# Kernel optimization log

Measured on AMD Instinct MI355X. Metric: run time of the kernel, lower is better.

Reference implementation:

```python
import jax, jax.numpy as jnp
import numpy as np

N, D, E, C = 8192, 64, 524288, 2


def setup_inputs() -> dict:
    key = jax.random.key(0)
    ks = jax.random.split(key, 14)
    src = jax.random.randint(ks[0], (E,), 0, N, dtype=jnp.int32)
    dst = jax.random.randint(ks[1], (E,), 0, N, dtype=jnp.int32)
    h = jax.random.normal(ks[2], (N, D), jnp.float32)
    # dense adjacency consistent with the edge list (A[u,v]=1 for edge u->v)
    one = jnp.ones((E,), jnp.float32)
    A = jnp.zeros((N, N), jnp.float32).at[src, dst].max(one)
    # motif adjacencies: random subsets of the base edges
    keep1 = jax.random.bernoulli(ks[3], 0.5, (E,)).astype(jnp.float32)
    keep2 = jax.random.bernoulli(ks[4], 0.3, (E,)).astype(jnp.float32)
    A1 = jnp.zeros((N, N), jnp.float32).at[src, dst].max(keep1)
    A2 = jnp.zeros((N, N), jnp.float32).at[src, dst].max(keep2)
    s = 0.05
    Ww = jax.random.normal(ks[5], (D, D), jnp.float32) * s
    Wb = jax.random.normal(ks[6], (D,), jnp.float32) * s
    fc0 = jax.random.normal(ks[7], (D, D), jnp.float32) * s
    fc1 = jax.random.normal(ks[8], (D, D), jnp.float32) * s
    fc2 = jax.random.normal(ks[9], (D, D), jnp.float32) * s
    lin_w = jax.random.normal(ks[10], (3 * D, C), jnp.float32) * s
    lin_b = jax.random.normal(ks[11], (C,), jnp.float32) * s
    return {"h": h, "A": A, "A1": A1, "A2": A2, "Ww": Ww, "Wb": Wb,
            "fc0": fc0, "fc1": fc1, "fc2": fc2, "lin_w": lin_w,
            "lin_b": lin_b, "src": src, "dst": dst}


def _dot_gat_pool(az, fc, src, dst, emask, nmask):
    # DGL DotGatConv (num_heads=1): ft = fc(az); e_uv = <ft_u, ft_v>/sqrt(F);
    # edge-softmax per destination; sum-aggregate; then avg-pool over subgraph nodes.
    n = az.shape[0]
    ft = az @ fc                                   # [N, F]
    scale = 1.0 / jnp.sqrt(jnp.float32(ft.shape[-1]))
    e = jnp.sum(ft[src] * ft[dst], axis=-1) * scale  # [E]
    neg = jnp.finfo(e.dtype).min
    e = jnp.where(emask, e, neg)
    m = jax.ops.segment_max(e, dst, num_segments=n)
    m = jnp.where(jnp.isfinite(m), m, 0.0)
    ex = jnp.where(emask, jnp.exp(e - m[dst]), 0.0)
    den = jax.ops.segment_sum(ex, dst, num_segments=n)
    alpha = ex / jnp.maximum(den[dst], 1e-9)       # [E]
    agg = jax.ops.segment_sum(alpha[:, None] * ft[src], dst, num_segments=n)  # [N, F]
    # mean over nodes present in the (motif) subgraph
    return jnp.sum(agg * nmask[:, None], axis=0) / jnp.maximum(jnp.sum(nmask), 1.0)


def reference(h, A, A1, A2, Ww, Wb, fc0, fc1, fc2, lin_w, lin_b, src, dst):
    n = h.shape[0]
    Z = (A @ h) @ Ww.T + Wb                        # Z = W(A h)
    outs = []
    # motif 0: full edge set, az = Z
    all_e = jnp.ones(src.shape, bool)
    all_n = jnp.ones((n,), jnp.float32)
    outs.append(_dot_gat_pool(Z, fc0, src, dst, all_e, all_n))
    # motifs 1, 2: edge subgraph where A_k[u, v] > 0, az = A_k @ Z
    for Ak, fck in ((A1, fc1), (A2, fc2)):
        emask = Ak[src, dst] > 0
        em = emask.astype(jnp.float32)
        nmask = jnp.zeros((n,), jnp.float32).at[src].max(em)
        nmask = jnp.maximum(nmask, jnp.zeros((n,), jnp.float32).at[dst].max(em))
        az = Ak @ Z
        outs.append(_dot_gat_pool(az, fck, src, dst, emask, nmask))
    feat = jnp.concatenate(outs)[None, :]          # [1, 3*F]
    return feat @ lin_w + lin_b                    # [1, num_classes]
```

## Files before the change

kernel.cpp:

```cpp
#include <hip/hip_runtime.h>

constexpr int N = 8192;
constexpr int D = 64;
constexpr int E = 524288;
constexpr int ND = N * D;

constexpr size_t SZ_BITMAP = (size_t)N * (size_t)N / 8;
constexpr size_t SZ_CNT    = 8256 * sizeof(int);
constexpr size_t O_BITMAP  = 0;
constexpr size_t O_SRCCNT  = O_BITMAP + SZ_BITMAP;
constexpr size_t O_DSTCNT  = O_SRCCNT + SZ_CNT;
constexpr size_t O_NF1     = O_DSTCNT + SZ_CNT;
constexpr size_t O_NF2     = O_NF1 + N;
constexpr size_t O_POOLED  = O_NF2 + N;
constexpr size_t ZERO_END  = O_POOLED + 1024;
constexpr size_t O_SRCPTR  = ZERO_END;
constexpr size_t O_DSTPTR  = O_SRCPTR + SZ_CNT;
constexpr size_t O_SRCFILL = O_DSTPTR + SZ_CNT;
constexpr size_t O_DSTFILL = O_SRCFILL + SZ_CNT;
constexpr size_t O_EFLAGS  = O_DSTFILL + SZ_CNT;
constexpr size_t O_CSRS    = O_EFLAGS + (size_t)E;
constexpr size_t O_CSRD    = O_CSRS + (size_t)E * 4;
constexpr size_t O_Z       = O_CSRD + (size_t)E * 4;
constexpr size_t O_FT      = O_Z + (size_t)N * D * 4;


__global__ void __launch_bounds__(256) edge_classify(
        const int* __restrict__ src, const int* __restrict__ dst,
        const float* __restrict__ A1, const float* __restrict__ A2,
        unsigned* __restrict__ bitmap,
        int* __restrict__ srcCnt, int* __restrict__ dstCnt,
        unsigned char* __restrict__ nf1, unsigned char* __restrict__ nf2,
        unsigned char* __restrict__ eflags) {
    int i = blockIdx.x * blockDim.x + threadIdx.x;
    if (i >= E) return;
    int u = src[i], v = dst[i];
    long long key = ((long long)u << 13) | v;
    unsigned bit = 1u << (key & 31);
    unsigned old = atomicOr(&bitmap[key >> 5], bit);
    int own = ((old & bit) == 0) ? 1 : 0;
    float a1 = A1[key];
    float a2 = A2[key];
    int f1 = (a1 > 0.0f) ? 1 : 0;
    int f2 = (a2 > 0.0f) ? 1 : 0;
    eflags[i] = (unsigned char)(own | (f1 << 1) | (f2 << 2));
    if (own) atomicAdd(&srcCnt[u], 1);
    atomicAdd(&dstCnt[v], 1);
    if (f1) { nf1[u] = 1; nf1[v] = 1; }
    if (f2) { nf2[u] = 1; nf2[v] = 1; }
}

__global__ void __launch_bounds__(256) scan2(
        const int* __restrict__ srcCnt, int* __restrict__ srcPtr, int* __restrict__ srcFill,
        const int* __restrict__ dstCnt, int* __restrict__ dstPtr, int* __restrict__ dstFill) {
    const int* cnt = (blockIdx.x == 0) ? srcCnt : dstCnt;
    int* ptr  = (blockIdx.x == 0) ? srcPtr : dstPtr;
    int* fill = (blockIdx.x == 0) ? srcFill : dstFill;
    __shared__ int ssum[256];
    int t = threadIdx.x;
    int base = t * 32;
    int loc[32];
    int s = 0;
    for (int j = 0; j < 32; ++j) { loc[j] = cnt[base + j]; s += loc[j]; }
    ssum[t] = s;
    __syncthreads();
    for (int off = 1; off < 256; off <<= 1) {
        int v = (t >= off) ? ssum[t - off] : 0;
        __syncthreads();
        ssum[t] += v;
        __syncthreads();
    }
    int ex = (t == 0) ? 0 : ssum[t - 1];
    for (int j = 0; j < 32; ++j) {
        ptr[base + j] = ex;
        fill[base + j] = ex;
        ex += loc[j];
    }
    if (t == 255) ptr[N] = ex;
}

__global__ void __launch_bounds__(256) csr_fill(
        const int* __restrict__ src, const int* __restrict__ dst,
        const unsigned char* __restrict__ eflags,
        int* __restrict__ srcFill, int* __restrict__ dstFill,
        int* __restrict__ csrS, int* __restrict__ csrD) {
    int i = blockIdx.x * blockDim.x + threadIdx.x;
    if (i >= E) return;
    int u = src[i], v = dst[i];
    int fl = eflags[i];
    int f12 = (fl >> 1) & 3;
    if (fl & 1) {
        int p = atomicAdd(&srcFill[u], 1);
        csrS[p] = v | (f12 << 13);
    }
    int p2 = atomicAdd(&dstFill[v], 1);
    csrD[p2] = u | (f12 << 13);
}

__global__ void __launch_bounds__(256) rowpipe1(
        const int* __restrict__ srcPtr, const int* __restrict__ csrS,
        const float* __restrict__ h, const float* __restrict__ Ww,
        const float* __restrict__ Wb, const float* __restrict__ fc0,
        float* __restrict__ Z, float* __restrict__ ft0) {
    __shared__ float W1[64 * 64];
    __shared__ float W2[64 * 64];
    int t = threadIdx.x;
    for (int i = t; i < 4096; i += 256) {
        int r = i >> 6, c = i & 63;
        W1[i] = Ww[c * 64 + r];
        W2[i] = fc0[i];
    }
    __syncthreads();
    int wid = t >> 6, lane = t & 63;
    int row = blockIdx.x * 4 + wid;
    int b = srcPtr[row], e = srcPtr[row + 1];
    float a0 = 0.0f, a1 = 0.0f, a2 = 0.0f, a3 = 0.0f;
    int j = b;
    for (; j + 3 < e; j += 4) {
        int u0 = csrS[j] & 8191, u1 = csrS[j + 1] & 8191;
        int u2 = csrS[j + 2] & 8191, u3 = csrS[j + 3] & 8191;
        a0 += h[(size_t)u0 * D + lane];
        a1 += h[(size_t)u1 * D + lane];
        a2 += h[(size_t)u2 * D + lane];
        a3 += h[(size_t)u3 * D + lane];
    }
    for (; j < e; ++j) a0 += h[(size_t)(csrS[j] & 8191) * D + lane];
    float ah = (a0 + a1) + (a2 + a3);
    float z = Wb[lane];
    #pragma unroll 8
    for (int k = 0; k < 64; ++k)
        z = fmaf(__shfl(ah, k), W1[k * 64 + lane], z);
    Z[(size_t)row * D + lane] = z;
    float f = 0.0f;
    #pragma unroll 8
    for (int k = 0; k < 64; ++k)
        f = fmaf(__shfl(z, k), W2[k * 64 + lane], f);
    ft0[(size_t)row * D + lane] = f;
}

__global__ void __launch_bounds__(256) rowpipe2(
        const int* __restrict__ srcPtr, const int* __restrict__ csrS,
        const float* __restrict__ Z,
        const float* __restrict__ fc1, const float* __restrict__ fc2,
        float* __restrict__ ft1, float* __restrict__ ft2) {
    __shared__ float W1[64 * 64];
    __shared__ float W2[64 * 64];
    int t = threadIdx.x;
    for (int i = t; i < 4096; i += 256) {
        W1[i] = fc1[i];
        W2[i] = fc2[i];
    }
    __syncthreads();
    int wid = t >> 6, lane = t & 63;
    int row = blockIdx.x * 4 + wid;
    int b = srcPtr[row], e = srcPtr[row + 1];
    float a1x = 0.0f, a2x = 0.0f, a1y = 0.0f, a2y = 0.0f;
    int j = b;
    for (; j + 1 < e; j += 2) {
        int e0 = csrS[j], e1 = csrS[j + 1];
        if (e0 >> 13) {
            float z = Z[(size_t)(e0 & 8191) * D + lane];
            if (e0 & (1 << 13)) a1x += z;
            if (e0 & (1 << 14)) a2x += z;
        }
        if (e1 >> 13) {
            float z = Z[(size_t)(e1 & 8191) * D + lane];
            if (e1 & (1 << 13)) a1y += z;
            if (e1 & (1 << 14)) a2y += z;
        }
    }
    for (; j < e; ++j) {
        int e0 = csrS[j];
        if (e0 >> 13) {
            float z = Z[(size_t)(e0 & 8191) * D + lane];
            if (e0 & (1 << 13)) a1x += z;
            if (e0 & (1 << 14)) a2x += z;
        }
    }
    float s1 = a1x + a1y, s2 = a2x + a2y;
    float f1 = 0.0f, f2 = 0.0f;
    #pragma unroll 8
    for (int k = 0; k < 64; ++k) {
        f1 = fmaf(__shfl(s1, k), W1[k * 64 + lane], f1);
        f2 = fmaf(__shfl(s2, k), W2[k * 64 + lane], f2);
    }
    ft1[(size_t)row * D + lane] = f1;
    ft2[(size_t)row * D + lane] = f2;
}

__global__ void __launch_bounds__(256) gat_fused_all(
        const float* __restrict__ ftAll, const int* __restrict__ dstPtr,
        const int* __restrict__ csrD, float* __restrict__ pooled) {
    int t = threadIdx.x, wid = t >> 6, lane = t & 63;
    int row = blockIdx.x * 4 + wid;
    __shared__ float fv[4][3][64];
    __shared__ float4 sw[4][64];
    __shared__ float red[3][256];
    const float* ft0 = ftAll;
    fv[wid][0][lane] = ft0[(size_t)row * D + lane];
    fv[wid][1][lane] = ft0[ND + (size_t)row * D + lane];
    fv[wid][2][lane] = ft0[2 * ND + (size_t)row * D + lane];
    const float4* fq0 = (const float4*)fv[wid][0];
    const float4* fq1 = (const float4*)fv[wid][1];
    const float4* fq2 = (const float4*)fv[wid][2];
    int b = dstPtr[row], e = dstPtr[row + 1];
    float mr0 = -3.0e38f, mr1 = -3.0e38f, mr2 = -3.0e38f;
    float den0 = 0.0f, den1 = 0.0f, den2 = 0.0f;
    float a0x = 0.0f, a0y = 0.0f, a1x = 0.0f, a1y = 0.0f, a2x = 0.0f, a2y = 0.0f;
    for (int cb = b; cb < e; cb += 64) {
        int j = cb + lane;
        bool valid = j < e;
        int ent = valid ? csrD[j] : 0;
        int u = ent & 8191;
        bool act1 = valid && (ent & (1 << 13));
        bool act2 = valid && (ent & (1 << 14));
        float s0 = -3.0e38f, s1 = -3.0e38f, s2 = -3.0e38f;
        const float4* pu = (const float4*)(ft0 + (size_t)u * D);
        if (valid) {
            float d0 = 0.0f, d1 = 0.0f;
            #pragma unroll
            for (int k = 0; k < 16; k += 2) {
                float4 a = pu[k], bq = fq0[k];
                float4 c = pu[k + 1], dq = fq0[k + 1];
                d0 = fmaf(a.x, bq.x, d0); d0 = fmaf(a.y, bq.y, d0);
                d0 = fmaf(a.z, bq.z, d0); d0 = fmaf(a.w, bq.w, d0);
                d1 = fmaf(c.x, dq.x, d1); d1 = fmaf(c.y, dq.y, d1);
                d1 = fmaf(c.z, dq.z, d1); d1 = fmaf(c.w, dq.w, d1);
            }
            s0 = (d0 + d1) * 0.125f;
        }
        if (act1) {
            const float4* p1 = pu + ND / 4;
            float d0 = 0.0f, d1 = 0.0f;
            #pragma unroll
            for (int k = 0; k < 16; k += 2) {
                float4 a = p1[k], bq = fq1[k];
                float4 c = p1[k + 1], dq = fq1[k + 1];
                d0 = fmaf(a.x, bq.x, d0); d0 = fmaf(a.y, bq.y, d0);
                d0 = fmaf(a.z, bq.z, d0); d0 = fmaf(a.w, bq.w, d0);
                d1 = fmaf(c.x, dq.x, d1); d1 = fmaf(c.y, dq.y, d1);
                d1 = fmaf(c.z, dq.z, d1); d1 = fmaf(c.w, dq.w, d1);
            }
            s1 = (d0 + d1) * 0.125f;
        }
        if (act2) {
            const float4* p2 = pu + 2 * (ND / 4);
            float d0 = 0.0f, d1 = 0.0f;
            #pragma unroll
            for (int k = 0; k < 16; k += 2) {
                float4 a = p2[k], bq = fq2[k];
                float4 c = p2[k + 1], dq = fq2[k + 1];
                d0 = fmaf(a.x, bq.x, d0); d0 = fmaf(a.y, bq.y, d0);
                d0 = fmaf(a.z, bq.z, d0); d0 = fmaf(a.w, bq.w, d0);
                d1 = fmaf(c.x, dq.x, d1); d1 = fmaf(c.y, dq.y, d1);
                d1 = fmaf(c.z, dq.z, d1); d1 = fmaf(c.w, dq.w, d1);
            }
            s2 = (d0 + d1) * 0.125f;
        }
        float c0 = s0, c1 = s1, c2 = s2;
        c0 = fmaxf(c0, __shfl_xor(c0, 1));  c1 = fmaxf(c1, __shfl_xor(c1, 1));  c2 = fmaxf(c2, __shfl_xor(c2, 1));
        c0 = fmaxf(c0, __shfl_xor(c0, 2));  c1 = fmaxf(c1, __shfl_xor(c1, 2));  c2 = fmaxf(c2, __shfl_xor(c2, 2));
        c0 = fmaxf(c0, __shfl_xor(c0, 4));  c1 = fmaxf(c1, __shfl_xor(c1, 4));  c2 = fmaxf(c2, __shfl_xor(c2, 4));
        c0 = fmaxf(c0, __shfl_xor(c0, 8));  c1 = fmaxf(c1, __shfl_xor(c1, 8));  c2 = fmaxf(c2, __shfl_xor(c2, 8));
        c0 = fmaxf(c0, __shfl_xor(c0, 16)); c1 = fmaxf(c1, __shfl_xor(c1, 16)); c2 = fmaxf(c2, __shfl_xor(c2, 16));
        c0 = fmaxf(c0, __shfl_xor(c0, 32)); c1 = fmaxf(c1, __shfl_xor(c1, 32)); c2 = fmaxf(c2, __shfl_xor(c2, 32));
        float nm0 = fmaxf(mr0, c0), nm1 = fmaxf(mr1, c1), nm2 = fmaxf(mr2, c2);
        float sc0 = __expf(mr0 - nm0), sc1 = __expf(mr1 - nm1), sc2 = __expf(mr2 - nm2);
        float w0 = valid ? __expf(s0 - nm0) : 0.0f;
        float w1 = act1 ? __expf(s1 - nm1) : 0.0f;
        float w2 = act2 ? __expf(s2 - nm2) : 0.0f;
        sw[wid][lane] = make_float4(w0, w1, w2, __int_as_float(u));
        float t0 = w0, t1 = w1, t2 = w2;
        t0 += __shfl_xor(t0, 1);  t1 += __shfl_xor(t1, 1);  t2 += __shfl_xor(t2, 1);
        t0 += __shfl_xor(t0, 2);  t1 += __shfl_xor(t1, 2);  t2 += __shfl_xor(t2, 2);
        t0 += __shfl_xor(t0, 4);  t1 += __shfl_xor(t1, 4);  t2 += __shfl_xor(t2, 4);
        t0 += __shfl_xor(t0, 8);  t1 += __shfl_xor(t1, 8);  t2 += __shfl_xor(t2, 8);
        t0 += __shfl_xor(t0, 16); t1 += __shfl_xor(t1, 16); t2 += __shfl_xor(t2, 16);
        t0 += __shfl_xor(t0, 32); t1 += __shfl_xor(t1, 32); t2 += __shfl_xor(t2, 32);
        den0 = den0 * sc0 + t0; den1 = den1 * sc1 + t1; den2 = den2 * sc2 + t2;
        a0x *= sc0; a0y *= sc0; a1x *= sc1; a1y *= sc1; a2x *= sc2; a2y *= sc2;
        mr0 = nm0; mr1 = nm1; mr2 = nm2;
        int csize = min(64, e - cb);
        const float* fbase = ft0 + lane;
        int q = 0;
        for (; q + 1 < csize; q += 2) {
            float4 e0 = sw[wid][q], e1 = sw[wid][q + 1];
            const float* p0 = fbase + (size_t)__float_as_int(e0.w) * D;
            const float* p1 = fbase + (size_t)__float_as_int(e1.w) * D;
            a0x = fmaf(e0.x, p0[0], a0x);
            a0y = fmaf(e1.x, p1[0], a0y);
            if (e0.y > 0.0f) a1x = fmaf(e0.y, p0[ND], a1x);
            if (e1.y > 0.0f) a1y = fmaf(e1.y, p1[ND], a1y);
            if (e0.z > 0.0f) a2x = fmaf(e0.z, p0[2 * ND], a2x);
            if (e1.z > 0.0f) a2y = fmaf(e1.z, p1[2 * ND], a2y);
        }
        if (q < csize) {
            float4 e0 = sw[wid][q];
            const float* p0 = fbase + (size_t)__float_as_int(e0.w) * D;
            a0x = fmaf(e0.x, p0[0], a0x);
            if (e0.y > 0.0f) a1x = fmaf(e0.y, p0[ND], a1x);
            if (e0.z > 0.0f) a2x = fmaf(e0.z, p0[2 * ND], a2x);
        }
    }
    red[0][t] = (a0x + a0y) / fmaxf(den0, 1e-9f);
    red[1][t] = (a1x + a1y) / fmaxf(den1, 1e-9f);
    red[2][t] = (a2x + a2y) / fmaxf(den2, 1e-9f);
    __syncthreads();
    if (wid < 3) {
        float s = red[wid][lane] + red[wid][64 + lane] + red[wid][128 + lane] + red[wid][192 + lane];
        atomicAdd(&pooled[wid * 64 + lane], s);
    }
}

__global__ void __launch_bounds__(256) final_kernel(
        const float* __restrict__ pooled,
        const unsigned char* __restrict__ nf1, const unsigned char* __restrict__ nf2,
        const float* __restrict__ lin_w, const float* __restrict__ lin_b,
        float* __restrict__ out) {
    __shared__ int r1[256], r2[256];
    __shared__ float feat[192];
    __shared__ int cnt[2];
    int t = threadIdx.x;
    int s1 = 0, s2 = 0;
    for (int i = t; i < N; i += 256) { s1 += nf1[i]; s2 += nf2[i]; }
    r1[t] = s1; r2[t] = s2;
    __syncthreads();
    for (int off = 128; off > 0; off >>= 1) {
        if (t < off) { r1[t] += r1[t + off]; r2[t] += r2[t + off]; }
        __syncthreads();
    }
    if (t == 0) { cnt[0] = r1[0]; cnt[1] = r2[0]; }
    __syncthreads();
    if (t < 192) {
        int sel = t >> 6;
        float div = (sel == 0) ? (float)N : fmaxf((float)cnt[sel - 1], 1.0f);
        feat[t] = pooled[t] / div;
    }
    __syncthreads();
    if (t < 2) {
        float o = lin_b[t];
        for (int k = 0; k < 192; ++k) o = fmaf(feat[k], lin_w[k * 2 + t], o);
        out[t] = o;
    }
}

extern "C" void kernel_launch(void* const* d_in, const int* in_sizes, int n_in,
                              void* d_out, int out_size, void* d_ws, size_t ws_size,
                              hipStream_t stream) {
    const float* h   = (const float*)d_in[0];
    const float* A1  = (const float*)d_in[2];
    const float* A2  = (const float*)d_in[3];
    const float* Ww  = (const float*)d_in[4];
    const float* Wb  = (const float*)d_in[5];
    const float* fc0 = (const float*)d_in[6];
    const float* fc1 = (const float*)d_in[7];
    const float* fc2 = (const float*)d_in[8];
    const float* lw  = (const float*)d_in[9];
    const float* lb  = (const float*)d_in[10];
    const int* src   = (const int*)d_in[11];
    const int* dst   = (const int*)d_in[12];
    float* out = (float*)d_out;

    char* w = (char*)d_ws;
    unsigned* bitmap   = (unsigned*)(w + O_BITMAP);
    int* srcCnt        = (int*)(w + O_SRCCNT);
    int* dstCnt        = (int*)(w + O_DSTCNT);
    unsigned char* nf1 = (unsigned char*)(w + O_NF1);
    unsigned char* nf2 = (unsigned char*)(w + O_NF2);
    float* pooled      = (float*)(w + O_POOLED);
    int* srcPtr        = (int*)(w + O_SRCPTR);
    int* dstPtr        = (int*)(w + O_DSTPTR);
    int* srcFill       = (int*)(w + O_SRCFILL);
    int* dstFill       = (int*)(w + O_DSTFILL);
    unsigned char* efl = (unsigned char*)(w + O_EFLAGS);
    int* csrS          = (int*)(w + O_CSRS);
    int* csrD          = (int*)(w + O_CSRD);
    float* Z           = (float*)(w + O_Z);
    float* ftAll       = (float*)(w + O_FT);
    float* ft1         = ftAll + (size_t)ND;
    float* ft2         = ftAll + 2 * (size_t)ND;

    hipMemsetAsync(w, 0, ZERO_END, stream);

    edge_classify<<<E / 256, 256, 0, stream>>>(src, dst, A1, A2, bitmap, srcCnt, dstCnt, nf1, nf2, efl);
    scan2<<<2, 256, 0, stream>>>(srcCnt, srcPtr, srcFill, dstCnt, dstPtr, dstFill);
    csr_fill<<<E / 256, 256, 0, stream>>>(src, dst, efl, srcFill, dstFill, csrS, csrD);

    rowpipe1<<<N / 4, 256, 0, stream>>>(srcPtr, csrS, h, Ww, Wb, fc0, Z, ftAll);
    rowpipe2<<<N / 4, 256, 0, stream>>>(srcPtr, csrS, Z, fc1, fc2, ft1, ft2);

    gat_fused_all<<<N / 4, 256, 0, stream>>>(ftAll, dstPtr, csrD, pooled);

    final_kernel<<<1, 256, 0, stream>>>(pooled, nf1, nf2, lw, lb, out);
}
```

Baseline: 842.7 us.

## Replace per-edge feature aggregation with per-source attention weights then dense pooling

Uses linearity of mean pooling: instead of gathering alpha-weighted ft[u] rows per destination, each edge atomically adds its normalized alpha into a per-source weight vector beta, and a separate dense kernel computes sum_u beta[u]*ft[u]. This removes the 64-wide per-edge feature gather in the GAT kernel, at the cost of a two-pass softmax (max then denominator), recomputing scores for rows with more than four chunks, scalar atomics on beta, and an extra launch plus zeroing a larger buffer.

```diff
diff --git a/kernel.cpp b/kernel.cpp
--- a/kernel.cpp
+++ b/kernel.cpp
@@ -13,7 +13,8 @@
 constexpr size_t O_NF1     = O_DSTCNT + SZ_CNT;
 constexpr size_t O_NF2     = O_NF1 + N;
 constexpr size_t O_POOLED  = O_NF2 + N;
-constexpr size_t ZERO_END  = O_POOLED + 1024;
+constexpr size_t O_BETA    = O_POOLED + 1024;
+constexpr size_t ZERO_END  = O_BETA + 3 * (size_t)N * 4;
 constexpr size_t O_SRCPTR  = ZERO_END;
 constexpr size_t O_DSTPTR  = O_SRCPTR + SZ_CNT;
 constexpr size_t O_SRCFILL = O_DSTPTR + SZ_CNT;
@@ -188,14 +189,64 @@
     ft2[(size_t)row * D + lane] = f2;
 }
 
-__global__ void __launch_bounds__(256) gat_fused_all(
+__device__ __forceinline__ void sddmm3(
+        const float* __restrict__ ft0,
+        const float4* __restrict__ fq0, const float4* __restrict__ fq1,
+        const float4* __restrict__ fq2,
+        int ent, bool valid, float& s0, float& s1, float& s2) {
+    s0 = -3.0e38f; s1 = -3.0e38f; s2 = -3.0e38f;
+    if (!valid) return;
+    int u = ent & 8191;
+    const float4* pu = (const float4*)(ft0 + (size_t)u * D);
+    {
+        float d0 = 0.0f, d1 = 0.0f;
+        #pragma unroll
+        for (int k = 0; k < 16; k += 2) {
+            float4 a = pu[k], bq = fq0[k];
+            float4 c = pu[k + 1], dq = fq0[k + 1];
+            d0 = fmaf(a.x, bq.x, d0); d0 = fmaf(a.y, bq.y, d0);
+            d0 = fmaf(a.z, bq.z, d0); d0 = fmaf(a.w, bq.w, d0);
+            d1 = fmaf(c.x, dq.x, d1); d1 = fmaf(c.y, dq.y, d1);
+            d1 = fmaf(c.z, dq.z, d1); d1 = fmaf(c.w, dq.w, d1);
+        }
+        s0 = (d0 + d1) * 0.125f;
+    }
+    if (ent & (1 << 13)) {
+        const float4* p1 = pu + ND / 4;
+        float d0 = 0.0f, d1 = 0.0f;
+        #pragma unroll
+        for (int k = 0; k < 16; k += 2) {
+            float4 a = p1[k], bq = fq1[k];
+            float4 c = p1[k + 1], dq = fq1[k + 1];
+            d0 = fmaf(a.x, bq.x, d0); d0 = fmaf(a.y, bq.y, d0);
+            d0 = fmaf(a.z, bq.z, d0); d0 = fmaf(a.w, bq.w, d0);
+            d1 = fmaf(c.x, dq.x, d1); d1 = fmaf(c.y, dq.y, d1);
+            d1 = fmaf(c.z, dq.z, d1); d1 = fmaf(c.w, dq.w, d1);
+        }
+        s1 = (d0 + d1) * 0.125f;
+    }
+    if (ent & (1 << 14)) {
+        const float4* p2 = pu + 2 * (ND / 4);
+        float d0 = 0.0f, d1 = 0.0f;
+        #pragma unroll
+        for (int k = 0; k < 16; k += 2) {
+            float4 a = p2[k], bq = fq2[k];
+            float4 c = p2[k + 1], dq = fq2[k + 1];
+            d0 = fmaf(a.x, bq.x, d0); d0 = fmaf(a.y, bq.y, d0);
+            d0 = fmaf(a.z, bq.z, d0); d0 = fmaf(a.w, bq.w, d0);
+            d1 = fmaf(c.x, dq.x, d1); d1 = fmaf(c.y, dq.y, d1);
+            d1 = fmaf(c.z, dq.z, d1); d1 = fmaf(c.w, dq.w, d1);
+        }
+        s2 = (d0 + d1) * 0.125f;
+    }
+}
+
+__global__ void __launch_bounds__(256) gat_alpha(
         const float* __restrict__ ftAll, const int* __restrict__ dstPtr,
-        const int* __restrict__ csrD, float* __restrict__ pooled) {
+        const int* __restrict__ csrD, float* __restrict__ beta) {
     int t = threadIdx.x, wid = t >> 6, lane = t & 63;
     int row = blockIdx.x * 4 + wid;
     __shared__ float fv[4][3][64];
-    __shared__ float4 sw[4][64];
-    __shared__ float red[3][256];
     const float* ft0 = ftAll;
     fv[wid][0][lane] = ft0[(size_t)row * D + lane];
     fv[wid][1][lane] = ft0[ND + (size_t)row * D + lane];
@@ -204,59 +255,17 @@
     const float4* fq1 = (const float4*)fv[wid][1];
     const float4* fq2 = (const float4*)fv[wid][2];
     int b = dstPtr[row], e = dstPtr[row + 1];
+    int nch = (e - b + 63) >> 6;
+    float w0r[4], w1r[4], w2r[4];
+    int entr[4];
     float mr0 = -3.0e38f, mr1 = -3.0e38f, mr2 = -3.0e38f;
-    float den0 = 0.0f, den1 = 0.0f, den2 = 0.0f;
-    float a0x = 0.0f, a0y = 0.0f, a1x = 0.0f, a1y = 0.0f, a2x = 0.0f, a2y = 0.0f;
-    for (int cb = b; cb < e; cb += 64) {
-        int j = cb + lane;
+    for (int c = 0; c < nch; ++c) {
+        int j = b + c * 64 + lane;
         bool valid = j < e;
-        int ent = valid ? csrD[j] : 0;
-        int u = ent & 8191;
-        bool act1 = valid && (ent & (1 << 13));
-        bool act2 = valid && (ent & (1 << 14));
-        float s0 = -3.0e38f, s1 = -3.0e38f, s2 = -3.0e38f;
-        const float4* pu = (const float4*)(ft0 + (size_t)u * D);
-        if (valid) {
-            float d0 = 0.0f, d1 = 0.0f;
-            #pragma unroll
-            for (int k = 0; k < 16; k += 2) {
-                float4 a = pu[k], bq = fq0[k];
-                float4 c = pu[k + 1], dq = fq0[k + 1];
-                d0 = fmaf(a.x, bq.x, d0); d0 = fmaf(a.y, bq.y, d0);
-                d0 = fmaf(a.z, bq.z, d0); d0 = fmaf(a.w, bq.w, d0);
-                d1 = fmaf(c.x, dq.x, d1); d1 = fmaf(c.y, dq.y, d1);
-                d1 = fmaf(c.z, dq.z, d1); d1 = fmaf(c.w, dq.w, d1);
-            }
-            s0 = (d0 + d1) * 0.125f;
-        }
-        if (act1) {
-            const float4* p1 = pu + ND / 4;
-            float d0 = 0.0f, d1 = 0.0f;
-            #pragma unroll
-            for (int k = 0; k < 16; k += 2) {
-                float4 a = p1[k], bq = fq1[k];
-                float4 c = p1[k + 1], dq = fq1[k + 1];
-                d0 = fmaf(a.x, bq.x, d0); d0 = fmaf(a.y, bq.y, d0);
-                d0 = fmaf(a.z, bq.z, d0); d0 = fmaf(a.w, bq.w, d0);
-                d1 = fmaf(c.x, dq.x, d1); d1 = fmaf(c.y, dq.y, d1);
-                d1 = fmaf(c.z, dq.z, d1); d1 = fmaf(c.w, dq.w, d1);
-            }
-            s1 = (d0 + d1) * 0.125f;
-        }
-        if (act2) {
-            const float4* p2 = pu + 2 * (ND / 4);
-            float d0 = 0.0f, d1 = 0.0f;
-            #pragma unroll
-            for (int k = 0; k < 16; k += 2) {
-                float4 a = p2[k], bq = fq2[k];
-                float4 c = p2[k + 1], dq = fq2[k + 1];
-                d0 = fmaf(a.x, bq.x, d0); d0 = fmaf(a.y, bq.y, d0);
-                d0 = fmaf(a.z, bq.z, d0); d0 = fmaf(a.w, bq.w, d0);
-                d1 = fmaf(c.x, dq.x, d1); d1 = fmaf(c.y, dq.y, d1);
-                d1 = fmaf(c.z, dq.z, d1); d1 = fmaf(c.w, dq.w, d1);
-            }
-            s2 = (d0 + d1) * 0.125f;
-        }
+        int ent = valid ? (csrD[j] | (1 << 15)) : 0;
+        float s0, s1, s2;
+        sddmm3(ft0, fq0, fq1, fq2, ent, valid, s0, s1, s2);
+        if (c < 4) { w0r[c] = s0; w1r[c] = s1; w2r[c] = s2; entr[c] = ent; }
         float c0 = s0, c1 = s1, c2 = s2;
         c0 = fmaxf(c0, __shfl_xor(c0, 1));  c1 = fmaxf(c1, __shfl_xor(c1, 1));  c2 = fmaxf(c2, __shfl_xor(c2, 1));
         c0 = fmaxf(c0, __shfl_xor(c0, 2));  c1 = fmaxf(c1, __shfl_xor(c1, 2));  c2 = fmaxf(c2, __shfl_xor(c2, 2));
@@ -264,12 +273,22 @@
         c0 = fmaxf(c0, __shfl_xor(c0, 8));  c1 = fmaxf(c1, __shfl_xor(c1, 8));  c2 = fmaxf(c2, __shfl_xor(c2, 8));
         c0 = fmaxf(c0, __shfl_xor(c0, 16)); c1 = fmaxf(c1, __shfl_xor(c1, 16)); c2 = fmaxf(c2, __shfl_xor(c2, 16));
         c0 = fmaxf(c0, __shfl_xor(c0, 32)); c1 = fmaxf(c1, __shfl_xor(c1, 32)); c2 = fmaxf(c2, __shfl_xor(c2, 32));
-        float nm0 = fmaxf(mr0, c0), nm1 = fmaxf(mr1, c1), nm2 = fmaxf(mr2, c2);
-        float sc0 = __expf(mr0 - nm0), sc1 = __expf(mr1 - nm1), sc2 = __expf(mr2 - nm2);
-        float w0 = valid ? __expf(s0 - nm0) : 0.0f;
-        float w1 = act1 ? __expf(s1 - nm1) : 0.0f;
-        float w2 = act2 ? __expf(s2 - nm2) : 0.0f;
-        sw[wid][lane] = make_float4(w0, w1, w2, __int_as_float(u));
+        mr0 = fmaxf(mr0, c0); mr1 = fmaxf(mr1, c1); mr2 = fmaxf(mr2, c2);
+    }
+    float den0 = 0.0f, den1 = 0.0f, den2 = 0.0f;
+    for (int c = 0; c < nch; ++c) {
+        float s0, s1, s2; int ent;
+        if (c < 4) { s0 = w0r[c]; s1 = w1r[c]; s2 = w2r[c]; ent = entr[c]; }
+        else {
+            int j = b + c * 64 + lane;
+            bool valid = j < e;
+            ent = valid ? (csrD[j] | (1 << 15)) : 0;
+            sddmm3(ft0, fq0, fq1, fq2, ent, valid, s0, s1, s2);
+        }
+        float w0 = (ent & (1 << 15)) ? __expf(s0 - mr0) : 0.0f;
+        float w1 = (ent & (1 << 13)) ? __expf(s1 - mr1) : 0.0f;
+        float w2 = (ent & (1 << 14)) ? __expf(s2 - mr2) : 0.0f;
+        if (c < 4) { w0r[c] = w0; w1r[c] = w1; w2r[c] = w2; }
         float t0 = w0, t1 = w1, t2 = w2;
         t0 += __shfl_xor(t0, 1);  t1 += __shfl_xor(t1, 1);  t2 += __shfl_xor(t2, 1);
         t0 += __shfl_xor(t0, 2);  t1 += __shfl_xor(t1, 2);  t2 += __shfl_xor(t2, 2);
@@ -277,34 +296,45 @@
         t0 += __shfl_xor(t0, 8);  t1 += __shfl_xor(t1, 8);  t2 += __shfl_xor(t2, 8);
         t0 += __shfl_xor(t0, 16); t1 += __shfl_xor(t1, 16); t2 += __shfl_xor(t2, 16);
         t0 += __shfl_xor(t0, 32); t1 += __shfl_xor(t1, 32); t2 += __shfl_xor(t2, 32);
-        den0 = den0 * sc0 + t0; den1 = den1 * sc1 + t1; den2 = den2 * sc2 + t2;
-        a0x *= sc0; a0y *= sc0; a1x *= sc1; a1y *= sc1; a2x *= sc2; a2y *= sc2;
-        mr0 = nm0; mr1 = nm1; mr2 = nm2;
-        int csize = min(64, e - cb);
-        const float* fbase = ft0 + lane;
-        int q = 0;
-        for (; q + 1 < csize; q += 2) {
-            float4 e0 = sw[wid][q], e1 = sw[wid][q + 1];
-            const float* p0 = fbase + (size_t)__float_as_int(e0.w) * D;
-            const float* p1 = fbase + (size_t)__float_as_int(e1.w) * D;
-            a0x = fmaf(e0.x, p0[0], a0x);
-            a0y = fmaf(e1.x, p1[0], a0y);
-            if (e0.y > 0.0f) a1x = fmaf(e0.y, p0[ND], a1x);
-            if (e1.y > 0.0f) a1y = fmaf(e1.y, p1[ND], a1y);
-            if (e0.z > 0.0f) a2x = fmaf(e0.z, p0[2 * ND], a2x);
-            if (e1.z > 0.0f) a2y = fmaf(e1.z, p1[2 * ND], a2y);
-        }
-        if (q < csize) {
-            float4 e0 = sw[wid][q];
-            const float* p0 = fbase + (size_t)__float_as_int(e0.w) * D;
-            a0x = fmaf(e0.x, p0[0], a0x);
-            if (e0.y > 0.0f) a1x = fmaf(e0.y, p0[ND], a1x);
-            if (e0.z > 0.0f) a2x = fmaf(e0.z, p0[2 * ND], a2x);
-        }
-    }
-    red[0][t] = (a0x + a0y) / fmaxf(den0, 1e-9f);
-    red[1][t] = (a1x + a1y) / fmaxf(den1, 1e-9f);
-    red[2][t] = (a2x + a2y) / fmaxf(den2, 1e-9f);
+        den0 += t0; den1 += t1; den2 += t2;
+    }
+    float i0 = 1.0f / fmaxf(den0, 1e-9f);
+    float i1 = 1.0f / fmaxf(den1, 1e-9f);
+    float i2 = 1.0f / fmaxf(den2, 1e-9f);
+    for (int c = 0; c < nch; ++c) {
+        float w0, w1, w2; int ent;
+        if (c < 4) { w0 = w0r[c]; w1 = w1r[c]; w2 = w2r[c]; ent = entr[c]; }
+        else {
+            int j = b + c * 64 + lane;
+            bool valid = j < e;
+            ent = valid ? (csrD[j] | (1 << 15)) : 0;
+            float s0, s1, s2;
+            sddmm3(ft0, fq0, fq1, fq2, ent, valid, s0, s1, s2);
+            w0 = (ent & (1 << 15)) ? __expf(s0 - mr0) : 0.0f;
+            w1 = (ent & (1 << 13)) ? __expf(s1 - mr1) : 0.0f;
+            w2 = (ent & (1 << 14)) ? __expf(s2 - mr2) : 0.0f;
+        }
+        int u = ent & 8191;
+        if (w0 > 0.0f) atomicAdd(&beta[u], w0 * i0);
+        if (w1 > 0.0f) atomicAdd(&beta[N + u], w1 * i1);
+        if (w2 > 0.0f) atomicAdd(&beta[2 * N + u], w2 * i2);
+    }
+}
+
+__global__ void __launch_bounds__(256) pool_dense(
+        const float* __restrict__ ftAll, const float* __restrict__ beta,
+        float* __restrict__ pooled) {
+    int t = threadIdx.x, wid = t >> 6, lane = t & 63;
+    float a0 = 0.0f, a1 = 0.0f, a2 = 0.0f;
+    for (int u = blockIdx.x * 4 + wid; u < N; u += gridDim.x * 4) {
+        float b0 = beta[u], b1 = beta[N + u], b2 = beta[2 * N + u];
+        const float* p = ftAll + (size_t)u * D + lane;
+        a0 = fmaf(b0, p[0], a0);
+        a1 = fmaf(b1, p[ND], a1);
+        a2 = fmaf(b2, p[2 * ND], a2);
+    }
+    __shared__ float red[3][256];
+    red[0][t] = a0; red[1][t] = a1; red[2][t] = a2;
     __syncthreads();
     if (wid < 3) {
         float s = red[wid][lane] + red[wid][64 + lane] + red[wid][128 + lane] + red[wid][192 + lane];
@@ -368,6 +398,7 @@
     unsigned char* nf1 = (unsigned char*)(w + O_NF1);
     unsigned char* nf2 = (unsigned char*)(w + O_NF2);
     float* pooled      = (float*)(w + O_POOLED);
+    float* beta        = (float*)(w + O_BETA);
     int* srcPtr        = (int*)(w + O_SRCPTR);
     int* dstPtr        = (int*)(w + O_DSTPTR);
     int* srcFill       = (int*)(w + O_SRCFILL);
@@ -389,7 +420,8 @@
     rowpipe1<<<N / 4, 256, 0, stream>>>(srcPtr, csrS, h, Ww, Wb, fc0, Z, ftAll);
     rowpipe2<<<N / 4, 256, 0, stream>>>(srcPtr, csrS, Z, fc1, fc2, ft1, ft2);
 
-    gat_fused_all<<<N / 4, 256, 0, stream>>>(ftAll, dstPtr, csrD, pooled);
+    gat_alpha<<<N / 4, 256, 0, stream>>>(ftAll, dstPtr, csrD, beta);
+    pool_dense<<<256, 256, 0, stream>>>(ftAll, beta, pooled);
 
     final_kernel<<<1, 256, 0, stream>>>(pooled, nf1, nf2, lw, lb, out);
 }
```

Result: no change. 831.5 us, median of 2 (-1.3%).
